# Optimization experiments

Measured on AMD Instinct MI355X. Metric: run time of the kernel, lower is better.

Reference implementation:

```python
import jax, jax.numpy as jnp
import numpy as np

N = 4_000_000  # observations
C = 2000       # cameras
B = 1000       # base poses
R = 8          # relative (rig) poses
P = 500_000    # 3D points


def quat_to_rotmat(q):
    # q: [..., 4] in pypose (x, y, z, w) order; normalized before use (as pypose does)
    q = q / jnp.linalg.norm(q, axis=-1, keepdims=True)
    x, y, z, w = q[..., 0], q[..., 1], q[..., 2], q[..., 3]
    r00 = 1 - 2 * (y * y + z * z); r01 = 2 * (x * y - w * z); r02 = 2 * (x * z + w * y)
    r10 = 2 * (x * y + w * z); r11 = 1 - 2 * (x * x + z * z); r12 = 2 * (y * z - w * x)
    r20 = 2 * (x * z - w * y); r21 = 2 * (y * z + w * x); r22 = 1 - 2 * (x * x + y * y)
    return jnp.stack([jnp.stack([r00, r01, r02], -1),
                      jnp.stack([r10, r11, r12], -1),
                      jnp.stack([r20, r21, r22], -1)], -2)


def setup_inputs() -> dict:
    key = jax.random.key(0)
    ks = jax.random.split(key, 10)
    cam = jax.random.randint(ks[0], (N,), 0, C)
    pt = jax.random.randint(ks[1], (N,), 0, P)
    pix = jax.random.normal(ks[2], (N, 2), dtype=jnp.float32) * 100.0 + 500.0
    observations = jnp.concatenate([cam[:, None].astype(jnp.float32),
                                    pt[:, None].astype(jnp.float32), pix], axis=1)
    # base poses: random rotation, translation near z=+10 so points project in front of camera
    tb = jax.random.normal(ks[3], (B, 3), dtype=jnp.float32) * 0.1 + jnp.array([0.0, 0.0, 10.0])
    qb = jax.random.normal(ks[4], (B, 4), dtype=jnp.float32)
    qb = qb / jnp.linalg.norm(qb, axis=-1, keepdims=True)
    base_poses = jnp.concatenate([tb, qb], axis=1)
    # relative poses: small rig offsets, near-identity rotation
    tr = jax.random.normal(ks[5], (R, 3), dtype=jnp.float32) * 0.05
    qr = jnp.concatenate([jax.random.normal(ks[6], (R, 3), dtype=jnp.float32) * 0.01,
                          jnp.ones((R, 1), jnp.float32)], axis=1)
    qr = qr / jnp.linalg.norm(qr, axis=-1, keepdims=True)
    relative_poses = jnp.concatenate([tr, qr], axis=1)
    points = jax.random.normal(ks[7], (P, 3), dtype=jnp.float32)
    # pinhole intrinsics K = [[f,0,cx],[0,f,cy],[0,0,1]]
    f = 1000.0 + jax.random.normal(ks[8], (C,), dtype=jnp.float32) * 10.0
    z = jnp.zeros((C,), jnp.float32); o = jnp.ones((C,), jnp.float32)
    cx = 500.0 * o; cy = 500.0 * o
    intrinsics = jnp.stack([jnp.stack([f, z, cx], -1),
                            jnp.stack([z, f, cy], -1),
                            jnp.stack([z, z, o], -1)], -2)
    base_idx = jax.random.randint(ks[9], (C,), 0, B)
    rel_idx = jax.random.randint(jax.random.fold_in(key, 11), (C,), 0, R)
    has_rel = jax.random.bernoulli(jax.random.fold_in(key, 12), 0.5, (C,))
    rel_idx = jnp.where(has_rel, rel_idx, -1)
    lookup_indices = jnp.stack([base_idx, rel_idx], axis=1).astype(jnp.int32)
    return {"observations": observations, "base_poses": base_poses,
            "relative_poses": relative_poses, "points": points,
            "intrinsics": intrinsics, "lookup_indices": lookup_indices}


def reference(observations, base_poses, relative_poses, points, intrinsics, lookup_indices):
    cam = observations[:, 0].astype(jnp.int32)
    pt = observations[:, 1].astype(jnp.int32)
    pixels_measured = observations[:, 2:]
    bpi = lookup_indices[cam, 0]          # [N]
    rpi = lookup_indices[cam, 1]          # [N], -1 means no relative pose
    mask = rpi != -1
    rel_safe = jnp.where(mask, rpi, 0)
    sel_base = base_poses[bpi]            # [N,7]
    t_base = sel_base[:, :3]
    R_base = quat_to_rotmat(sel_base[:, 3:])  # [N,3,3]
    sel_rel = relative_poses[rel_safe]    # [N,7]
    t_rel = sel_rel[:, :3]
    R_rel = quat_to_rotmat(sel_rel[:, 3:])
    R_comp = jnp.einsum('nij,njk->nik', R_base, R_rel)
    t_comp = t_base + jnp.einsum('nij,nj->ni', R_base, t_rel)
    R_final = jnp.where(mask[:, None, None], R_comp, R_base)
    t_final = jnp.where(mask[:, None], t_comp, t_base)
    p_cam = jnp.einsum('nij,nj->ni', R_final, points[pt]) + t_final
    proj = jnp.einsum('nij,nj->ni', intrinsics[cam], p_cam)
    pred = proj[:, :2] / proj[:, 2:3]
    return (pred - pixels_measured).ravel()
```

## Files before the change

### kernel.cpp

```cpp
#include <hip/hip_runtime.h>
#include <hip/hip_fp16.h>
#include <math.h>

#define C_MAX 2000
#define DEPTH 8
#define TPB 512

typedef float f32x4 __attribute__((ext_vector_type(4)));

__device__ __forceinline__ unsigned pkh(float a, float b) {
    union { unsigned u; __half2 h; } x;
    x.h = __floats2half2_rn(a, b);
    return x.u;
}
__device__ __forceinline__ float2 uph(unsigned u) {
    union { unsigned u; __half2 h; } x;
    x.u = u;
    return make_float2(__low2float(x.h), __high2float(x.h));
}

__device__ __forceinline__ void quat_to_R(float q0, float q1, float q2, float q3, float R[9]) {
    float inv = 1.0f / sqrtf(q0 * q0 + q1 * q1 + q2 * q2 + q3 * q3);
    float x = q0 * inv, y = q1 * inv, z = q2 * inv, w = q3 * inv;
    R[0] = 1.0f - 2.0f * (y * y + z * z);
    R[1] = 2.0f * (x * y - w * z);
    R[2] = 2.0f * (x * z + w * y);
    R[3] = 2.0f * (x * y + w * z);
    R[4] = 1.0f - 2.0f * (x * x + z * z);
    R[5] = 2.0f * (y * z - w * x);
    R[6] = 2.0f * (x * z - w * y);
    R[7] = 2.0f * (y * z + w * x);
    R[8] = 1.0f - 2.0f * (x * x + y * y);
}

__global__ void cam_precompute(const float* __restrict__ base_poses,
                               const float* __restrict__ rel_poses,
                               const float* __restrict__ intr,
                               const int* __restrict__ lookup,
                               uint4* __restrict__ cam4,
                               uint2* __restrict__ cam2,
                               int C) {
    int c = blockIdx.x * blockDim.x + threadIdx.x;
    if (c >= C) return;
    int bpi = lookup[2 * c + 0];
    int rpi = lookup[2 * c + 1];
    bool has_rel = (rpi != -1);
    int rs = has_rel ? rpi : 0;

    const float* bp = base_poses + 7 * bpi;
    float tb0 = bp[0], tb1 = bp[1], tb2 = bp[2];
    float Rb[9];
    quat_to_R(bp[3], bp[4], bp[5], bp[6], Rb);

    const float* rp = rel_poses + 7 * rs;
    float Rr[9];
    quat_to_R(rp[3], rp[4], rp[5], rp[6], Rr);

    float Rf[9], tf0, tf1, tf2;
    if (has_rel) {
        #pragma unroll
        for (int i = 0; i < 3; ++i) {
            #pragma unroll
            for (int j = 0; j < 3; ++j) {
                Rf[3 * i + j] = Rb[3 * i + 0] * Rr[0 + j]
                              + Rb[3 * i + 1] * Rr[3 + j]
                              + Rb[3 * i + 2] * Rr[6 + j];
            }
        }
        tf0 = tb0 + Rb[0] * rp[0] + Rb[1] * rp[1] + Rb[2] * rp[2];
        tf1 = tb1 + Rb[3] * rp[0] + Rb[4] * rp[1] + Rb[5] * rp[2];
        tf2 = tb2 + Rb[6] * rp[0] + Rb[7] * rp[1] + Rb[8] * rp[2];
    } else {
        #pragma unroll
        for (int i = 0; i < 9; ++i) Rf[i] = Rb[i];
        tf0 = tb0; tf1 = tb1; tf2 = tb2;
    }

    const float* K = intr + 9 * c;
    float M[9], v[3];
    #pragma unroll
    for (int i = 0; i < 3; ++i) {
        #pragma unroll
        for (int j = 0; j < 3; ++j) {
            M[3 * i + j] = K[3 * i + 0] * Rf[0 + j]
                         + K[3 * i + 1] * Rf[3 + j]
                         + K[3 * i + 2] * Rf[6 + j];
        }
        v[i] = K[3 * i + 0] * tf0 + K[3 * i + 1] * tf1 + K[3 * i + 2] * tf2;
    }

    uint4 w0;
    uint2 w1;
    w0.x = pkh(M[0], M[1]);
    w0.y = pkh(M[2], M[3]);
    w0.z = pkh(M[4], M[5]);
    w0.w = pkh(M[6], M[7]);
    w1.x = pkh(M[8], v[0]);
    w1.y = pkh(v[1], v[2]);
    cam4[c] = w0;
    cam2[c] = w1;
}

__global__ void pack_points(const float* __restrict__ pts, uint2* __restrict__ ph, int P) {
    int i = blockIdx.x * blockDim.x + threadIdx.x;
    if (i < P) {
        float x = pts[3 * i + 0], y = pts[3 * i + 1], z = pts[3 * i + 2];
        uint2 q;
        q.x = pkh(x, y);
        q.y = pkh(z, 0.0f);
        ph[i] = q;
    }
}

__device__ __forceinline__ float2 project_one(const uint4& A, const uint2& B,
                                              const uint2& q, float mx, float my) {
    float2 m01 = uph(A.x);
    float2 m23 = uph(A.y);
    float2 m45 = uph(A.z);
    float2 m67 = uph(A.w);
    float2 m8v0 = uph(B.x);
    float2 v12 = uph(B.y);
    float2 xy = uph(q.x);
    float2 zp = uph(q.y);
    float px = xy.x, py = xy.y, pz = zp.x;

    float jx = m01.x * px + m01.y * py + m23.x * pz + m8v0.y;
    float jy = m23.y * px + m45.x * py + m45.y * pz + v12.x;
    float jz = m67.x * px + m67.y * py + m8v0.x * pz + v12.y;
    float iz = 1.0f / jz;
    return make_float2(jx * iz - mx, jy * iz - my);
}

typedef float f32x2 __attribute__((ext_vector_type(2)));

__launch_bounds__(TPB, 4)
__global__ void residual_ws(const f32x4* __restrict__ obsv,
                            const uint2* __restrict__ pts,
                            const uint4* __restrict__ cam4g,
                            const uint2* __restrict__ cam2g,
                            float2* __restrict__ out,
                            long N,
                            int C) {
    __shared__ uint4 s4[C_MAX];
    __shared__ uint2 s2[C_MAX];
    for (int i = threadIdx.x; i < C; i += blockDim.x) {
        s4[i] = cam4g[i];
        s2[i] = cam2g[i];
    }
    __syncthreads();

    const long CHUNK = (long)TPB * DEPTH;
    long blockBase = (long)blockIdx.x * CHUNK;
    int wave = threadIdx.x >> 6;
    int lane = threadIdx.x & 63;
    long base = blockBase + (long)wave * (64 * DEPTH) + lane;

    if (blockBase + CHUNK <= N) {
        f32x4 o[DEPTH];
        #pragma unroll
        for (int k = 0; k < DEPTH; ++k)
            o[k] = __builtin_nontemporal_load(&obsv[base + 64 * k]);

        int ci[DEPTH], pi[DEPTH];
        #pragma unroll
        for (int k = 0; k < DEPTH; ++k) {
            ci[k] = (int)o[k].x;
            pi[k] = (int)o[k].y;
        }

        uint2 q[DEPTH];
        #pragma unroll
        for (int k = 0; k < DEPTH; ++k) q[k] = pts[pi[k]];

        uint4 A[DEPTH];
        uint2 B[DEPTH];
        #pragma unroll
        for (int k = 0; k < DEPTH; ++k) {
            A[k] = s4[ci[k]];
            B[k] = s2[ci[k]];
        }

        __builtin_amdgcn_sched_barrier(0);

        #pragma unroll
        for (int k = 0; k < DEPTH; ++k) {
            float2 r = project_one(A[k], B[k], q[k], o[k].z, o[k].w);
            f32x2 w = {r.x, r.y};
            __builtin_nontemporal_store(w, (f32x2*)&out[base + 64 * k]);
        }
    } else {
        for (long i = blockBase + threadIdx.x; i < N; i += TPB) {
            f32x4 ob = obsv[i];
            int c = (int)ob.x;
            int pt = (int)ob.y;
            uint4 A = s4[c];
            uint2 B = s2[c];
            uint2 q = pts[pt];
            float2 r = project_one(A, B, q, ob.z, ob.w);
            out[i] = r;
        }
    }
}

extern "C" void kernel_launch(void* const* d_in, const int* in_sizes, int n_in,
                              void* d_out, int out_size, void* d_ws, size_t ws_size,
                              hipStream_t stream) {
    const float* obs = (const float*)d_in[0];
    const float* base_poses = (const float*)d_in[1];
    const float* rel_poses = (const float*)d_in[2];
    const float* points = (const float*)d_in[3];
    const float* intr = (const float*)d_in[4];
    const int* lookup = (const int*)d_in[5];

    long N = in_sizes[0] / 4;
    int P = in_sizes[3] / 3;
    int C = in_sizes[5] / 2;

    uint4* cam4 = (uint4*)d_ws;
    uint2* cam2 = (uint2*)((char*)d_ws + (size_t)C_MAX * 16);
    uint2* pts_h = (uint2*)((char*)d_ws + (size_t)C_MAX * 24);

    cam_precompute<<<(C + 255) / 256, 256, 0, stream>>>(
        base_poses, rel_poses, intr, lookup, cam4, cam2, C);
    pack_points<<<(P + 255) / 256, 256, 0, stream>>>(points, pts_h, P);

    long CHUNK = (long)TPB * DEPTH;
    int blocks = (int)((N + CHUNK - 1) / CHUNK);
    residual_ws<<<blocks, TPB, 0, stream>>>(
        (const f32x4*)obs, pts_h, cam4, cam2, (float2*)d_out, N, C);
}
```

Baseline: 52.77 us.

## Use fixed grid with balanced per-block ranges and looping residual kernel

Replaces the one-chunk-per-block grid with a fixed number of blocks, each looping over an evenly sized contiguous range of observations with per-element validity masking. This is meant to amortize the per-block shared-memory camera table load and avoid a tail wave, and it raises the occupancy hint in launch bounds. The risks are a partially filled final iteration per block, a tighter register budget, and a changed memory access pattern.

```diff
diff --git a/kernel.cpp b/kernel.cpp
--- a/kernel.cpp
+++ b/kernel.cpp
@@ -5,8 +5,10 @@
 #define C_MAX 2000
 #define DEPTH 8
 #define TPB 512
+#define NBLOCKS 768
 
 typedef float f32x4 __attribute__((ext_vector_type(4)));
+typedef float f32x2 __attribute__((ext_vector_type(2)));
 
 __device__ __forceinline__ unsigned pkh(float a, float b) {
     union { unsigned u; __half2 h; } x;
@@ -131,16 +133,15 @@
     return make_float2(jx * iz - mx, jy * iz - my);
 }
 
-typedef float f32x2 __attribute__((ext_vector_type(2)));
-
-__launch_bounds__(TPB, 4)
-__global__ void residual_ws(const f32x4* __restrict__ obsv,
-                            const uint2* __restrict__ pts,
-                            const uint4* __restrict__ cam4g,
-                            const uint2* __restrict__ cam2g,
-                            float2* __restrict__ out,
-                            long N,
-                            int C) {
+__launch_bounds__(TPB, 6)
+__global__ void residual_bal(const f32x4* __restrict__ obsv,
+                             const uint2* __restrict__ pts,
+                             const uint4* __restrict__ cam4g,
+                             const uint2* __restrict__ cam2g,
+                             float2* __restrict__ out,
+                             long N,
+                             int C,
+                             long per_block) {
     __shared__ uint4 s4[C_MAX];
     __shared__ uint2 s2[C_MAX];
     for (int i = threadIdx.x; i < C; i += blockDim.x) {
@@ -149,17 +150,22 @@
     }
     __syncthreads();
 
-    const long CHUNK = (long)TPB * DEPTH;
-    long blockBase = (long)blockIdx.x * CHUNK;
-    int wave = threadIdx.x >> 6;
-    int lane = threadIdx.x & 63;
-    long base = blockBase + (long)wave * (64 * DEPTH) + lane;
-
-    if (blockBase + CHUNK <= N) {
+    long r0 = (long)blockIdx.x * per_block;
+    long r1 = r0 + per_block;
+    if (r1 > N) r1 = N;
+    if (r0 >= r1) return;
+
+    for (long i0 = r0 + threadIdx.x; i0 < r1; i0 += (long)TPB * DEPTH) {
+        int valmask = 0;
         f32x4 o[DEPTH];
         #pragma unroll
-        for (int k = 0; k < DEPTH; ++k)
-            o[k] = __builtin_nontemporal_load(&obsv[base + 64 * k]);
+        for (int k = 0; k < DEPTH; ++k) {
+            long idx = i0 + (long)k * TPB;
+            bool val = idx < r1;
+            valmask |= (val ? 1 : 0) << k;
+            long safe = val ? idx : r0;
+            o[k] = __builtin_nontemporal_load(&obsv[safe]);
+        }
 
         int ci[DEPTH], pi[DEPTH];
         #pragma unroll
@@ -185,19 +191,10 @@
         #pragma unroll
         for (int k = 0; k < DEPTH; ++k) {
             float2 r = project_one(A[k], B[k], q[k], o[k].z, o[k].w);
-            f32x2 w = {r.x, r.y};
-            __builtin_nontemporal_store(w, (f32x2*)&out[base + 64 * k]);
-        }
-    } else {
-        for (long i = blockBase + threadIdx.x; i < N; i += TPB) {
-            f32x4 ob = obsv[i];
-            int c = (int)ob.x;
-            int pt = (int)ob.y;
-            uint4 A = s4[c];
-            uint2 B = s2[c];
-            uint2 q = pts[pt];
-            float2 r = project_one(A, B, q, ob.z, ob.w);
-            out[i] = r;
+            if (valmask & (1 << k)) {
+                f32x2 w = {r.x, r.y};
+                __builtin_nontemporal_store(w, (f32x2*)&out[i0 + (long)k * TPB]);
+            }
         }
     }
 }
@@ -224,8 +221,7 @@
         base_poses, rel_poses, intr, lookup, cam4, cam2, C);
     pack_points<<<(P + 255) / 256, 256, 0, stream>>>(points, pts_h, P);
 
-    long CHUNK = (long)TPB * DEPTH;
-    int blocks = (int)((N + CHUNK - 1) / CHUNK);
-    residual_ws<<<blocks, TPB, 0, stream>>>(
-        (const f32x4*)obs, pts_h, cam4, cam2, (float2*)d_out, N, C);
-}
+    long per_block = (N + (long)NBLOCKS * 64 - 1) / ((long)NBLOCKS * 64) * 64;
+    residual_bal<<<NBLOCKS, TPB, 0, stream>>>(
+        (const f32x4*)obs, pts_h, cam4, cam2, (float2*)d_out, N, C, per_block);
+}
```

New measurement: 72.61 us. +37.6%, slower.

## Use persistent balanced blocks that loop over contiguous observation ranges

Applied to the files above, without the earlier changes.

Replaces the one-chunk-per-block grid (about 977 blocks of 4096 observations) with a fixed set of about 768 blocks, each handling an equal contiguous range. Each block walks its range in depth-8 passes and finishes with depth-4/2/1 passes and a scalar remainder. The intent is to pay the per-block shared-memory load of the camera table fewer times and to balance work across the CUs. The cost is a serial loop inside each block, so there is less memory-level parallelism across blocks and the tail passes have shallower prefetch depth.

```diff
diff --git a/kernel.cpp b/kernel.cpp
--- a/kernel.cpp
+++ b/kernel.cpp
@@ -3,10 +3,11 @@
 #include <math.h>
 
 #define C_MAX 2000
-#define DEPTH 8
 #define TPB 512
+#define NBLOCKS 768
 
 typedef float f32x4 __attribute__((ext_vector_type(4)));
+typedef float f32x2 __attribute__((ext_vector_type(2)));
 
 __device__ __forceinline__ unsigned pkh(float a, float b) {
     union { unsigned u; __half2 h; } x;
@@ -131,16 +132,60 @@
     return make_float2(jx * iz - mx, jy * iz - my);
 }
 
-typedef float f32x2 __attribute__((ext_vector_type(2)));
+template <int D>
+__device__ __forceinline__ void pass(long i, int wave, int lane,
+                                     const f32x4* __restrict__ obsv,
+                                     const uint2* __restrict__ pts,
+                                     const uint4* s4, const uint2* s2,
+                                     float2* __restrict__ out) {
+    long base = i + (long)wave * (64 * D) + lane;
+
+    f32x4 o[D];
+    #pragma unroll
+    for (int k = 0; k < D; ++k)
+        o[k] = __builtin_nontemporal_load(&obsv[base + 64 * k]);
+
+    int ci[D], pi[D];
+    #pragma unroll
+    for (int k = 0; k < D; ++k) {
+        ci[k] = (int)o[k].x;
+        pi[k] = (int)o[k].y;
+    }
+
+    uint2 q[D];
+    #pragma unroll
+    for (int k = 0; k < D; ++k) q[k] = pts[pi[k]];
+
+    uint4 A[D];
+    uint2 B[D];
+    #pragma unroll
+    for (int k = 0; k < D; ++k) {
+        A[k] = s4[ci[k]];
+        B[k] = s2[ci[k]];
+    }
+
+    __builtin_amdgcn_sched_barrier(0);
+
+    #pragma unroll
+    for (int k = 0; k < D; ++k) {
+        float2 r = project_one(A[k], B[k], q[k], o[k].z, o[k].w);
+        f32x2 w = {r.x, r.y};
+        __builtin_nontemporal_store(w, (f32x2*)&out[base + 64 * k]);
+    }
+}
 
 __launch_bounds__(TPB, 4)
-__global__ void residual_ws(const f32x4* __restrict__ obsv,
-                            const uint2* __restrict__ pts,
-                            const uint4* __restrict__ cam4g,
-                            const uint2* __restrict__ cam2g,
-                            float2* __restrict__ out,
-                            long N,
-                            int C) {
+__global__ void residual_bal2(const f32x4* __restrict__ obsv,
+                              const uint2* __restrict__ pts,
+                              const uint4* __restrict__ cam4g,
+                              const uint2* __restrict__ cam2g,
+                              float2* __restrict__ out,
+                              long N,
+                              int C,
+                              long per_block) {
+    long r0 = (long)blockIdx.x * per_block;
+    if (r0 >= N) return;
+
     __shared__ uint4 s4[C_MAX];
     __shared__ uint2 s2[C_MAX];
     for (int i = threadIdx.x; i < C; i += blockDim.x) {
@@ -149,56 +194,36 @@
     }
     __syncthreads();
 
-    const long CHUNK = (long)TPB * DEPTH;
-    long blockBase = (long)blockIdx.x * CHUNK;
+    long r1 = r0 + per_block;
+    if (r1 > N) r1 = N;
+
     int wave = threadIdx.x >> 6;
     int lane = threadIdx.x & 63;
-    long base = blockBase + (long)wave * (64 * DEPTH) + lane;
-
-    if (blockBase + CHUNK <= N) {
-        f32x4 o[DEPTH];
-        #pragma unroll
-        for (int k = 0; k < DEPTH; ++k)
-            o[k] = __builtin_nontemporal_load(&obsv[base + 64 * k]);
-
-        int ci[DEPTH], pi[DEPTH];
-        #pragma unroll
-        for (int k = 0; k < DEPTH; ++k) {
-            ci[k] = (int)o[k].x;
-            pi[k] = (int)o[k].y;
-        }
-
-        uint2 q[DEPTH];
-        #pragma unroll
-        for (int k = 0; k < DEPTH; ++k) q[k] = pts[pi[k]];
-
-        uint4 A[DEPTH];
-        uint2 B[DEPTH];
-        #pragma unroll
-        for (int k = 0; k < DEPTH; ++k) {
-            A[k] = s4[ci[k]];
-            B[k] = s2[ci[k]];
-        }
-
-        __builtin_amdgcn_sched_barrier(0);
-
-        #pragma unroll
-        for (int k = 0; k < DEPTH; ++k) {
-            float2 r = project_one(A[k], B[k], q[k], o[k].z, o[k].w);
-            f32x2 w = {r.x, r.y};
-            __builtin_nontemporal_store(w, (f32x2*)&out[base + 64 * k]);
-        }
-    } else {
-        for (long i = blockBase + threadIdx.x; i < N; i += TPB) {
-            f32x4 ob = obsv[i];
-            int c = (int)ob.x;
-            int pt = (int)ob.y;
-            uint4 A = s4[c];
-            uint2 B = s2[c];
-            uint2 q = pts[pt];
-            float2 r = project_one(A, B, q, ob.z, ob.w);
-            out[i] = r;
-        }
+
+    long i = r0;
+    for (; i + (long)TPB * 8 <= r1; i += (long)TPB * 8)
+        pass<8>(i, wave, lane, obsv, pts, s4, s2, out);
+    if (i + (long)TPB * 4 <= r1) {
+        pass<4>(i, wave, lane, obsv, pts, s4, s2, out);
+        i += (long)TPB * 4;
+    }
+    if (i + (long)TPB * 2 <= r1) {
+        pass<2>(i, wave, lane, obsv, pts, s4, s2, out);
+        i += (long)TPB * 2;
+    }
+    if (i + (long)TPB <= r1) {
+        pass<1>(i, wave, lane, obsv, pts, s4, s2, out);
+        i += (long)TPB;
+    }
+    for (long j = i + threadIdx.x; j < r1; j += TPB) {
+        f32x4 ob = obsv[j];
+        int c = (int)ob.x;
+        int pt = (int)ob.y;
+        uint4 A = s4[c];
+        uint2 B = s2[c];
+        uint2 q = pts[pt];
+        float2 r = project_one(A, B, q, ob.z, ob.w);
+        out[j] = r;
     }
 }
 
@@ -224,8 +249,9 @@
         base_poses, rel_poses, intr, lookup, cam4, cam2, C);
     pack_points<<<(P + 255) / 256, 256, 0, stream>>>(points, pts_h, P);
 
-    long CHUNK = (long)TPB * DEPTH;
-    int blocks = (int)((N + CHUNK - 1) / CHUNK);
-    residual_ws<<<blocks, TPB, 0, stream>>>(
-        (const f32x4*)obs, pts_h, cam4, cam2, (float2*)d_out, N, C);
-}
+    long per_block = (N + (long)NBLOCKS - 1) / NBLOCKS;
+    per_block = (per_block + 63) / 64 * 64;
+    int blocks = (int)((N + per_block - 1) / per_block);
+    residual_bal2<<<blocks, TPB, 0, stream>>>(
+        (const f32x4*)obs, pts_h, cam4, cam2, (float2*)d_out, N, C, per_block);
+}
```

Measured after the change: 53.52 us. Within noise of the previous version (+1.4%).
